# Kernel optimization log

Hardware: AMD Instinct MI355X
Metric: run time of the kernel (lower is better)

## Reference

```python
import jax, jax.numpy as jnp
import numpy as np

N_USERS = 65536
N_ENT = 8192
C = 64
N_REL = 16
E = 1000000
NNZ = 1000000
LAMBDA_COEFF = 0.5
EPS = 1e-12


def setup_inputs() -> dict:
    key = jax.random.key(0)
    ks = jax.random.split(key, 8)
    return {
        "user_emb": jax.random.normal(ks[0], (N_USERS, C), jnp.float32) * 0.1,
        "entity_emb": jax.random.normal(ks[1], (N_ENT, C), jnp.float32) * 0.1,
        "weight": jax.random.normal(ks[2], (N_REL - 1, C), jnp.float32) * 0.1,
        "edge_index": jax.random.randint(ks[3], (2, E), 0, N_ENT, dtype=jnp.int32),
        "edge_type": jax.random.randint(ks[4], (E,), 1, N_REL, dtype=jnp.int32),
        "interact_rows": jax.random.randint(ks[5], (NNZ,), 0, N_USERS, dtype=jnp.int32),
        "interact_cols": jax.random.randint(ks[6], (NNZ,), 0, N_ENT, dtype=jnp.int32),
        "interact_vals": jax.random.uniform(ks[7], (NNZ,), jnp.float32),
        "n_hops": 2,
        "topk": 10,
    }


def _l2_normalize(x):
    # F.normalize(p=2, dim=1) with eps=1e-12
    n = jnp.linalg.norm(x, axis=-1, keepdims=True)
    return x / jnp.maximum(n, EPS)


def _build_adj_dense(context, topk):
    # cosine-sim kNN graph + symmetric normalization, returned dense [n, n]
    n = context.shape[0]
    cn = context / jnp.linalg.norm(context, axis=-1, keepdims=True)
    sim = cn @ cn.T                                  # [n, n]
    knn_val, knn_ind = jax.lax.top_k(sim, topk)      # [n, k]
    rowsum = knn_val.sum(-1)                         # sparse rowsum per row
    d = rowsum ** -0.5                               # D^{-1/2}
    vals = d[:, None] * knn_val * d[knn_ind]         # D^-1/2 A D^-1/2 values
    rows = jnp.broadcast_to(jnp.arange(n)[:, None], (n, topk))
    return jnp.zeros((n, n), context.dtype).at[rows, knn_ind].add(vals)


def _aggregate(entity_emb, user_emb, head, tail, edge_type,
               interact_rows, interact_cols, interact_vals, weight):
    rel = weight[edge_type - 1]                      # [E, C]
    neigh = entity_emb[tail] * rel                   # [E, C]
    # per-edge attention: (||h*r||_2 * ||t*r||_2)^2  -> scalar per edge
    s = (jnp.linalg.norm(entity_emb[head] * rel, axis=1)
         * jnp.linalg.norm(neigh, axis=1)) ** 2      # [E]
    # scatter_softmax over edges grouped by head
    smax = jax.ops.segment_max(s, head, num_segments=N_ENT)
    ex = jnp.exp(s - smax[head])
    denom = jax.ops.segment_sum(ex, head, num_segments=N_ENT)
    w = ex / denom[head]                             # [E]
    entity_agg = jax.ops.segment_sum(neigh * w[:, None], head, num_segments=N_ENT)
    # user_agg = interact_mat @ entity_emb (sparse COO mm)
    user_agg = jax.ops.segment_sum(interact_vals[:, None] * entity_emb[interact_cols],
                                   interact_rows, num_segments=N_USERS)
    score = jax.nn.softmax(user_emb @ weight.T, axis=-1)   # [n_users, n_rel-1]
    user_agg = user_agg + (score @ weight) * user_agg
    return entity_agg, user_agg


def reference(user_emb, entity_emb, weight, edge_index, edge_type,
              interact_rows, interact_cols, interact_vals, n_hops, topk):
    head, tail = edge_index[0], edge_index[1]
    origin_item_adj = _build_adj_dense(entity_emb, topk)
    entity_res = entity_emb
    user_res = user_emb
    ent, usr = entity_emb, user_emb
    for _ in range(n_hops):
        ent, usr = _aggregate(ent, usr, head, tail, edge_type,
                              interact_rows, interact_cols, interact_vals, weight)
        ent = _l2_normalize(ent)
        usr = _l2_normalize(usr)
        entity_res = entity_res + ent
        user_res = user_res + usr
    item_adj = (1.0 - LAMBDA_COEFF) * _build_adj_dense(entity_res, topk) \
               + LAMBDA_COEFF * origin_item_adj
    return entity_res, user_res, item_adj
```

## Files before the change

### kernel.cpp

```cpp
#include <hip/hip_runtime.h>
#include <math.h>
#include <float.h>

#define N_USERS 65536
#define N_ENT   8192
#define CDIM    64
#define N_RELM1 15
#define E_EDGES 1000000
#define NNZV    1000000
#define TOPK    10
#define NCAND   12
#define EPSN    1e-12f

typedef float f32x4 __attribute__((ext_vector_type(4)));
typedef short short8 __attribute__((ext_vector_type(8)));

__device__ inline unsigned umaxu(unsigned a, unsigned b){ return a > b ? a : b; }
__device__ inline unsigned uminu(unsigned a, unsigned b){ return a < b ? a : b; }

__device__ inline float wred_sum(float v){
#pragma unroll
  for (int m = 32; m; m >>= 1) v += __shfl_xor(v, m, 64);
  return v;
}
__device__ inline float wred_max(float v){
#pragma unroll
  for (int m = 32; m; m >>= 1) v = fmaxf(v, __shfl_xor(v, m, 64));
  return v;
}

__device__ inline unsigned bf16_rne(float x){
  unsigned u = __float_as_uint(x);
  return (u + 0x7FFFu + ((u >> 16) & 1u)) >> 16;
}

__global__ __launch_bounds__(256) void k_prep(const float* __restrict__ x, float* __restrict__ cn,
                                              short* __restrict__ hi_p, short* __restrict__ lo_p,
                                              const float* __restrict__ wmat, float* __restrict__ nsq,
                                              int do_nsq){
  __shared__ float wl[N_RELM1 * CDIM];
  int tid = threadIdx.x;
  if (do_nsq){
    for (int t = tid; t < N_RELM1 * CDIM; t += 256) wl[t] = wmat[t];
  }
  __syncthreads();
  int w = blockIdx.x * 4 + (tid >> 6);
  int k = tid & 63;
  float v = x[w * CDIM + k];
  float ss = wred_sum(v * v);
  float cv = v / sqrtf(ss);
  cn[w * CDIM + k] = cv;
  unsigned h = bf16_rne(cv);
  float hf = __uint_as_float(h << 16);
  unsigned l2 = bf16_rne(cv - hf);
  int T = w >> 4, c = w & 15;
  int f = k >> 5, q = (k >> 3) & 3, j = k & 7;
  size_t a = ((size_t)(T * 2 + f) * 64 + q * 16 + c) * 8 + j;
  hi_p[a] = (short)h;
  lo_p[a] = (short)l2;
  if (do_nsq){
    float out = 0.f;
    for (int r = 0; r < N_RELM1; ++r){
      float t = v * wl[r * CDIM + k];
      float s2 = wred_sum(t * t);
      if (k == r) out = s2;
    }
    if (k < N_RELM1) nsq[w * N_RELM1 + k] = out;
  }
}

__global__ __launch_bounds__(256) void k_sim_topk(const short* __restrict__ hi_p,
                                                  const short* __restrict__ lo_p,
                                                  unsigned* __restrict__ keys){
  const int tid = threadIdx.x;
  const int w = tid >> 6, l = tid & 63;
  const int c = l & 15, q = l >> 4;
  const int rowset = (w >> 1) << 4;
  const int half = w & 1;
  const int cy = blockIdx.y;
  const int row0 = blockIdx.x * 32 + rowset;
  const int R = row0 >> 4;

  const short8* H8 = (const short8*)hi_p;
  const short8* L8 = (const short8*)lo_p;

  const short8 a_hi0 = H8[(size_t)R * 128 + l];
  const short8 a_hi1 = H8[(size_t)R * 128 + 64 + l];
  const short8 a_lo0 = L8[(size_t)R * 128 + l];
  const short8 a_lo1 = L8[(size_t)R * 128 + 64 + l];

  unsigned key[4][8];
#pragma unroll
  for (int s = 0; s < 4; ++s)
#pragma unroll
    for (int t = 0; t < 8; ++t) key[s][t] = 0u;

  const f32x4 z4 = {0.f, 0.f, 0.f, 0.f};
  const int bt = cy * 256 + half * 128;
#pragma unroll 2
  for (int lt = 0; lt < 128; ++lt){
    const size_t bo = (size_t)(bt + lt) * 128 + l;
    short8 b_hi0 = H8[bo];
    short8 b_hi1 = H8[bo + 64];
    short8 b_lo0 = L8[bo];
    short8 b_lo1 = L8[bo + 64];
    f32x4 p0 = __builtin_amdgcn_mfma_f32_16x16x32_bf16(a_hi0, b_hi0, z4, 0, 0, 0);
    f32x4 p1 = __builtin_amdgcn_mfma_f32_16x16x32_bf16(a_hi0, b_lo0, z4, 0, 0, 0);
    f32x4 p2 = __builtin_amdgcn_mfma_f32_16x16x32_bf16(a_lo0, b_hi0, z4, 0, 0, 0);
    p0 = __builtin_amdgcn_mfma_f32_16x16x32_bf16(a_hi1, b_hi1, p0, 0, 0, 0);
    p1 = __builtin_amdgcn_mfma_f32_16x16x32_bf16(a_hi1, b_lo1, p1, 0, 0, 0);
    p2 = __builtin_amdgcn_mfma_f32_16x16x32_bf16(a_lo1, b_hi1, p2, 0, 0, 0);
#pragma unroll
    for (int s = 0; s < 4; ++s){
      float v = p0[s] + p1[s] + p2[s];
      unsigned u = __float_as_uint(v);
      unsigned kk = ((u ^ (unsigned)(((int)u >> 31) | 0x80000000)) & 0xFFFFFF00u) | (unsigned)lt;
#pragma unroll
      for (int i = 7; i >= 1; --i)
        key[s][i] = umaxu(uminu(key[s][i - 1], kk), key[s][i]);
      key[s][0] = umaxu(key[s][0], kk);
    }
  }

#pragma unroll
  for (int s = 0; s < 4; ++s){
    int grow = row0 + 4 * q + s;
    unsigned* kp = keys + ((size_t)grow * 64 + (size_t)(cy * 32 + half * 16 + c)) * 8;
    ((uint4*)kp)[0] = (uint4){key[s][0], key[s][1], key[s][2], key[s][3]};
    ((uint4*)kp)[1] = (uint4){key[s][4], key[s][5], key[s][6], key[s][7]};
  }
}

__global__ __launch_bounds__(256) void k_refine(const float* __restrict__ cn,
                                                const unsigned* __restrict__ keys,
                                                float* __restrict__ kv, int* __restrict__ ki,
                                                float* __restrict__ dvec){
  int row = blockIdx.x * 4 + (threadIdx.x >> 6);
  int l = threadIdx.x & 63;
  const unsigned* kp = keys + ((size_t)row * 64 + l) * 8;
  uint4 k0 = ((const uint4*)kp)[0], k1 = ((const uint4*)kp)[1];
  unsigned kk0 = k0.x, kk1 = k0.y, kk2 = k0.z, kk3 = k0.w;
  unsigned kk4 = k1.x, kk5 = k1.y, kk6 = k1.z, kk7 = k1.w;
  const int cbase = (l >> 5) * 4096 + ((l >> 4) & 1) * 2048 + (l & 15);

  int ji[NCAND];
#pragma unroll
  for (int t = 0; t < NCAND; ++t){
    unsigned bk = kk0;
    int myc = cbase + (int)(kk0 & 0xFFu) * 16;
    int bc = myc;
#pragma unroll
    for (int m = 32; m; m >>= 1){
      unsigned ok = (unsigned)__shfl_xor((int)bk, m, 64);
      int oc = __shfl_xor(bc, m, 64);
      if (ok > bk || (ok == bk && oc < bc)){ bk = ok; bc = oc; }
    }
    if (kk0 == bk && myc == bc){
      kk0 = kk1; kk1 = kk2; kk2 = kk3; kk3 = kk4; kk4 = kk5; kk5 = kk6; kk6 = kk7; kk7 = 0u;
    }
    ji[t] = bc;
  }

  float v = cn[(size_t)row * CDIM + l];
  float dv[NCAND];
#pragma unroll
  for (int t = 0; t < NCAND; ++t)
    dv[t] = wred_sum(v * cn[(size_t)ji[t] * CDIM + l]);

  unsigned used = 0;
  float rs = 0.f;
  for (int k = 0; k < TOPK; ++k){
    float bv = -FLT_MAX; int bi = 0x7FFFFFFF; int bs = 0;
#pragma unroll
    for (int t = 0; t < NCAND; ++t){
      if (used & (1u << t)) continue;
      if (dv[t] > bv || (dv[t] == bv && ji[t] < bi)){ bv = dv[t]; bi = ji[t]; bs = t; }
    }
    used |= 1u << bs; rs += bv;
    if (l == 0){ kv[(size_t)row * TOPK + k] = bv; ki[(size_t)row * TOPK + k] = bi; }
  }
  if (l == 0) dvec[row] = 1.0f / sqrtf(rs);
}

__global__ void k_hist2(const int* __restrict__ head, const int* __restrict__ irows,
                        int* __restrict__ cnt_all){
  int e = blockIdx.x * blockDim.x + threadIdx.x;
  if (e < E_EDGES)                  atomicAdd(&cnt_all[head[e]], 1);
  else if (e < E_EDGES + NNZV)      atomicAdd(&cnt_all[N_ENT + irows[e - E_EDGES]], 1);
}

__global__ __launch_bounds__(1024) void k_scan_local2(const int* __restrict__ cnt_all,
                                                      int* __restrict__ rp_grp,
                                                      int* __restrict__ rp_int,
                                                      int* __restrict__ part){
  __shared__ int sh[1024];
  int b = blockIdx.x, tid = threadIdx.x;
  int src = (b < 8) ? (b * 1024 + tid) : (N_ENT + (b - 8) * 1024 + tid);
  int v = cnt_all[src];
  sh[tid] = v; __syncthreads();
  for (int off = 1; off < 1024; off <<= 1){
    int t = (tid >= off) ? sh[tid - off] : 0;
    __syncthreads();
    sh[tid] += t;
    __syncthreads();
  }
  int ex = sh[tid] - v;
  if (b < 8) rp_grp[b * 1024 + tid] = ex;
  else       rp_int[(b - 8) * 1024 + tid] = ex;
  if (tid == 1023) part[b] = sh[1023];
}

__global__ void k_scan_part2(int* __restrict__ part){
  int wid = threadIdx.x >> 6, lane = threadIdx.x & 63;
  if (wid == 0){
    int v = (lane < 8) ? part[lane] : 0;
    int orig = v;
    for (int off = 1; off < 64; off <<= 1){ int t = __shfl_up(v, off, 64); if (lane >= off) v += t; }
    if (lane < 8) part[lane] = v - orig;
  } else {
    int v = part[8 + lane];
    int orig = v;
    for (int off = 1; off < 64; off <<= 1){ int t = __shfl_up(v, off, 64); if (lane >= off) v += t; }
    part[8 + lane] = v - orig;
  }
}

__global__ __launch_bounds__(1024) void k_scan_add2(int* __restrict__ rp_grp, int* __restrict__ rp_int,
                                                    const int* __restrict__ part,
                                                    int* __restrict__ wk_grp, int* __restrict__ wk_int){
  int b = blockIdx.x, tid = threadIdx.x;
  if (b < 8){
    int g = b * 1024 + tid;
    int v = rp_grp[g] + part[b];
    rp_grp[g] = v; wk_grp[g] = v;
  } else {
    int g = (b - 8) * 1024 + tid;
    int v = rp_int[g] + part[b];
    rp_int[g] = v; wk_int[g] = v;
  }
  if (b == 0 && tid == 0){ rp_grp[N_ENT] = E_EDGES; rp_int[N_USERS] = NNZV; }
}

__global__ void k_scatter2(const int* __restrict__ head, const int* __restrict__ tail,
                           const int* __restrict__ etype,
                           const int* __restrict__ irows, const int* __restrict__ icols,
                           const float* __restrict__ ivals,
                           int* __restrict__ wk_grp, int* __restrict__ wk_int,
                           int* __restrict__ pack, int* __restrict__ ocol, float* __restrict__ oval){
  int e = blockIdx.x * blockDim.x + threadIdx.x;
  if (e < E_EDGES){
    int h = head[e];
    int pos = atomicAdd(&wk_grp[h], 1);
    pack[pos] = tail[e] | ((etype[e] - 1) << 16);
  } else if (e < E_EDGES + NNZV){
    int ee = e - E_EDGES;
    int r = irows[ee];
    int pos = atomicAdd(&wk_int[r], 1);
    ocol[pos] = icols[ee];
    oval[pos] = ivals[ee];
  }
}

__global__ __launch_bounds__(256) void k_entity_hop(const float* __restrict__ ent_cur,
                                                    const float* __restrict__ nsq,
                                                    const float* __restrict__ wmat,
                                                    const int* __restrict__ rowptr,
                                                    const int* __restrict__ pack,
                                                    float* __restrict__ ent_next,
                                                    float* __restrict__ nsq_next,
                                                    float* __restrict__ res, int hop0){
  __shared__ float wl[N_RELM1 * CDIM];
  int tid = threadIdx.x;
  for (int t = tid; t < N_RELM1 * CDIM; t += 256) wl[t] = wmat[t];
  __syncthreads();
  int i = blockIdx.x * 4 + (tid >> 6);
  int lane = tid & 63;
  int beg = rowptr[i], end = rowptr[i + 1];

  float sm = 0.f;
  for (int p = beg + lane; p < end; p += 64){
    int pk = pack[p]; int t = pk & 0xFFFF; int r = pk >> 16;
    sm = fmaxf(sm, nsq[i * N_RELM1 + r] * nsq[t * N_RELM1 + r]);
  }
  sm = wred_max(sm);

  float acc = 0.f, dsum = 0.f;
  for (int base = beg; base < end; base += 64){
    int p = base + lane;
    int pk = (p < end) ? pack[p] : 0;
    int t = pk & 0xFFFF; int r = pk >> 16;
    float s = nsq[i * N_RELM1 + r] * nsq[t * N_RELM1 + r];
    float e = (p < end) ? __expf(s - sm) : 0.f;
    dsum += e;
    int cnt = end - base; if (cnt > 64) cnt = 64;
#pragma unroll 8
    for (int qq = 0; qq < cnt; ++qq){
      float eq = __shfl(e, qq, 64);
      int tq = __shfl(t, qq, 64);
      int rq = __shfl(r, qq, 64);
      acc = fmaf(eq * wl[rq * CDIM + lane], ent_cur[(size_t)tq * CDIM + lane], acc);
    }
  }
  float denom = wred_sum(dsum);

  float agg = (end > beg) ? acc / denom : 0.f;
  float nrm = sqrtf(wred_sum(agg * agg));
  float out = agg / fmaxf(nrm, EPSN);
  if (hop0){
    ent_next[(size_t)i * CDIM + lane] = out;
    res[(size_t)i * CDIM + lane] = ent_cur[(size_t)i * CDIM + lane] + out;
    float o = 0.f;
    for (int r = 0; r < N_RELM1; ++r){
      float t = out * wl[r * CDIM + lane];
      float s2 = wred_sum(t * t);
      if (lane == r) o = s2;
    }
    if (lane < N_RELM1) nsq_next[i * N_RELM1 + lane] = o;
  } else {
    res[(size_t)i * CDIM + lane] += out;
  }
}

__global__ __launch_bounds__(256) void k_user_hop(const float* __restrict__ base,
                                                  const float* __restrict__ ent_cur,
                                                  const float* __restrict__ wmat,
                                                  const int* __restrict__ rowptr,
                                                  const int* __restrict__ cols,
                                                  const float* __restrict__ vals,
                                                  float* __restrict__ res, int hop0){
  __shared__ float wl[N_RELM1 * CDIM];
  int tid = threadIdx.x;
  for (int t = tid; t < N_RELM1 * CDIM; t += 256) wl[t] = wmat[t];
  __syncthreads();
  int u = blockIdx.x * 4 + (tid >> 6);
  int lane = tid & 63;
  float bv = base[(size_t)u * CDIM + lane];
  float rprev = hop0 ? bv : res[(size_t)u * CDIM + lane];
  float uv = hop0 ? bv : (rprev - bv);

  float dr[N_RELM1];
#pragma unroll
  for (int r = 0; r < N_RELM1; ++r) dr[r] = wred_sum(uv * wl[r * CDIM + lane]);
  float mx = dr[0];
#pragma unroll
  for (int r = 1; r < N_RELM1; ++r) mx = fmaxf(mx, dr[r]);
  float se = 0.f;
#pragma unroll
  for (int r = 0; r < N_RELM1; ++r){ dr[r] = __expf(dr[r] - mx); se += dr[r]; }
  float m = 0.f;
#pragma unroll
  for (int r = 0; r < N_RELM1; ++r) m = fmaf(dr[r], wl[r * CDIM + lane], m);
  m /= se;

  int beg = rowptr[u], end = rowptr[u + 1];
  float acc = 0.f;
#pragma unroll 4
  for (int p = beg; p < end; ++p)
    acc = fmaf(vals[p], ent_cur[(size_t)cols[p] * CDIM + lane], acc);

  float u2 = acc * (1.f + m);
  float nrm = sqrtf(wred_sum(u2 * u2));
  float out = u2 / fmaxf(nrm, EPSN);
  res[(size_t)u * CDIM + lane] = rprev + out;
}

__global__ void k_scatter_adj2(const float* __restrict__ kv0, const int* __restrict__ ki0,
                               const float* __restrict__ d0,
                               const float* __restrict__ kv2, const int* __restrict__ ki2,
                               const float* __restrict__ d2,
                               float* __restrict__ adj){
  int g = blockIdx.x * blockDim.x + threadIdx.x;
  const int n = N_ENT * TOPK;
  if (g < n){
    int i = g / TOPK; int j = ki0[g];
    atomicAdd(&adj[(size_t)i * N_ENT + j], 0.5f * d0[i] * kv0[g] * d0[j]);
  } else if (g < 2 * n){
    int gg = g - n;
    int i = gg / TOPK; int j = ki2[gg];
    atomicAdd(&adj[(size_t)i * N_ENT + j], 0.5f * d2[i] * kv2[gg] * d2[j]);
  }
}

extern "C" void kernel_launch(void* const* d_in, const int* in_sizes, int n_in,
                              void* d_out, int out_size, void* d_ws, size_t ws_size,
                              hipStream_t stream){
  const float* user_emb   = (const float*)d_in[0];
  const float* entity_emb = (const float*)d_in[1];
  const float* weight     = (const float*)d_in[2];
  const int*   head       = (const int*)d_in[3];
  const int*   tail       = head + E_EDGES;
  const int*   etype      = (const int*)d_in[4];
  const int*   irows      = (const int*)d_in[5];
  const int*   icols      = (const int*)d_in[6];
  const float* ivals      = (const float*)d_in[7];

  float* out_ent = (float*)d_out;
  float* out_usr = out_ent + (size_t)N_ENT * CDIM;
  float* out_adj = out_usr + (size_t)N_USERS * CDIM;

  char* W = (char*)d_ws;
  size_t off = 0;
  auto alloc = [&](size_t bytes) -> char* {
    char* p = W + off;
    off = (off + bytes + 1023) & ~(size_t)1023;
    return p;
  };
  float* cn       = (float*)alloc((size_t)N_ENT * CDIM * 4);
  short* cn_hi    = (short*)alloc((size_t)N_ENT * CDIM * 2);
  short* cn_lo    = (short*)alloc((size_t)N_ENT * CDIM * 2);
  unsigned* skeys = (unsigned*)alloc((size_t)N_ENT * 64 * 8 * 4);
  float* kv0      = (float*)alloc((size_t)N_ENT * TOPK * 4);
  int*   ki0      = (int*)  alloc((size_t)N_ENT * TOPK * 4);
  float* kv2      = (float*)alloc((size_t)N_ENT * TOPK * 4);
  int*   ki2      = (int*)  alloc((size_t)N_ENT * TOPK * 4);
  float* d0       = (float*)alloc((size_t)N_ENT * 4);
  float* d2       = (float*)alloc((size_t)N_ENT * 4);
  float* nsq_a    = (float*)alloc((size_t)N_ENT * N_RELM1 * 4);
  float* nsq_b    = (float*)alloc((size_t)N_ENT * N_RELM1 * 4);
  float* ent_a    = (float*)alloc((size_t)N_ENT * CDIM * 4);
  int*   cnt_all  = (int*)  alloc((size_t)(N_ENT + N_USERS) * 4);
  int*   rp_grp   = (int*)  alloc((size_t)(N_ENT + 1) * 4);
  int*   wk_grp   = (int*)  alloc((size_t)N_ENT * 4);
  int*   grp_pack = (int*)  alloc((size_t)E_EDGES * 4);
  int*   rp_int   = (int*)  alloc((size_t)(N_USERS + 1) * 4);
  int*   wk_int   = (int*)  alloc((size_t)N_USERS * 4);
  int*   int_col  = (int*)  alloc((size_t)NNZV * 4);
  float* int_val  = (float*)alloc((size_t)NNZV * 4);
  int*   part     = (int*)  alloc(128 * 4);

  const int TOT = E_EDGES + NNZV;
  const int TB  = (TOT + 255) / 256;

  hipMemsetAsync(cnt_all, 0, (size_t)(N_ENT + N_USERS) * 4, stream);
  k_hist2<<<TB, 256, 0, stream>>>(head, irows, cnt_all);
  k_scan_local2<<<72, 1024, 0, stream>>>(cnt_all, rp_grp, rp_int, part);
  k_scan_part2<<<1, 128, 0, stream>>>(part);
  k_scan_add2<<<72, 1024, 0, stream>>>(rp_grp, rp_int, part, wk_grp, wk_int);
  k_scatter2<<<TB, 256, 0, stream>>>(head, tail, etype, irows, icols, ivals,
                                     wk_grp, wk_int, grp_pack, int_col, int_val);

  k_prep<<<N_ENT / 4, 256, 0, stream>>>(entity_emb, cn, cn_hi, cn_lo, weight, nsq_a, 1);
  k_sim_topk<<<dim3(N_ENT / 32, 2), 256, 0, stream>>>(cn_hi, cn_lo, skeys);
  k_refine<<<N_ENT / 4, 256, 0, stream>>>(cn, skeys, kv0, ki0, d0);

  k_entity_hop<<<N_ENT / 4, 256, 0, stream>>>(entity_emb, nsq_a, weight, rp_grp, grp_pack,
                                              ent_a, nsq_b, out_ent, 1);
  k_user_hop<<<N_USERS / 4, 256, 0, stream>>>(user_emb, entity_emb, weight, rp_int,
                                              int_col, int_val, out_usr, 1);

  k_entity_hop<<<N_ENT / 4, 256, 0, stream>>>(ent_a, nsq_b, weight, rp_grp, grp_pack,
                                              ent_a, nsq_b, out_ent, 0);
  k_user_hop<<<N_USERS / 4, 256, 0, stream>>>(user_emb, ent_a, weight, rp_int,
                                              int_col, int_val, out_usr, 0);

  k_prep<<<N_ENT / 4, 256, 0, stream>>>(out_ent, cn, cn_hi, cn_lo, weight, nsq_a, 0);
  k_sim_topk<<<dim3(N_ENT / 32, 2), 256, 0, stream>>>(cn_hi, cn_lo, skeys);
  k_refine<<<N_ENT / 4, 256, 0, stream>>>(cn, skeys, kv2, ki2, d2);

  hipMemsetAsync(out_adj, 0, (size_t)N_ENT * N_ENT * 4, stream);
  k_scatter_adj2<<<(2 * N_ENT * TOPK + 255) / 256, 256, 0, stream>>>(kv0, ki0, d0, kv2, ki2, d2, out_adj);
}
```

Measured before the change: 1.032 ms.

## Use single-bf16 similarity, privatized histogram/scatter counters, and fused adjacency zero-write

The candidate similarity screen now uses one bf16 MFMA product instead of the three-term hi/lo split, and the exact fp32 refine pass widens from 12 to 16 candidates to make up for the lower screening precision. The edge/interaction histogram and scatter atomics are spread over 8 block-indexed counter copies to cut atomic contention, with the scan extended to produce per-copy cursors. The separate memset plus scatter kernel for the dense adjacency is replaced by one kernel per row that zeroes the row and then adds its top-k entries. The risk is that a true top-10 neighbour falls outside the 16 bf16-ranked candidates.

```diff
diff --git a/kernel.cpp b/kernel.cpp
--- a/kernel.cpp
+++ b/kernel.cpp
@@ -9,7 +9,8 @@
 #define E_EDGES 1000000
 #define NNZV    1000000
 #define TOPK    10
-#define NCAND   12
+#define NCAND   16
+#define KTOT    (N_ENT + N_USERS)
 #define EPSN    1e-12f
 
 typedef float f32x4 __attribute__((ext_vector_type(4)));
@@ -35,7 +36,7 @@
 }
 
 __global__ __launch_bounds__(256) void k_prep(const float* __restrict__ x, float* __restrict__ cn,
-                                              short* __restrict__ hi_p, short* __restrict__ lo_p,
+                                              short* __restrict__ hi_p,
                                               const float* __restrict__ wmat, float* __restrict__ nsq,
                                               int do_nsq){
   __shared__ float wl[N_RELM1 * CDIM];
@@ -51,13 +52,10 @@
   float cv = v / sqrtf(ss);
   cn[w * CDIM + k] = cv;
   unsigned h = bf16_rne(cv);
-  float hf = __uint_as_float(h << 16);
-  unsigned l2 = bf16_rne(cv - hf);
   int T = w >> 4, c = w & 15;
   int f = k >> 5, q = (k >> 3) & 3, j = k & 7;
   size_t a = ((size_t)(T * 2 + f) * 64 + q * 16 + c) * 8 + j;
   hi_p[a] = (short)h;
-  lo_p[a] = (short)l2;
   if (do_nsq){
     float out = 0.f;
     for (int r = 0; r < N_RELM1; ++r){
@@ -70,7 +68,6 @@
 }
 
 __global__ __launch_bounds__(256) void k_sim_topk(const short* __restrict__ hi_p,
-                                                  const short* __restrict__ lo_p,
                                                   unsigned* __restrict__ keys){
   const int tid = threadIdx.x;
   const int w = tid >> 6, l = tid & 63;
@@ -82,12 +79,9 @@
   const int R = row0 >> 4;
 
   const short8* H8 = (const short8*)hi_p;
-  const short8* L8 = (const short8*)lo_p;
 
   const short8 a_hi0 = H8[(size_t)R * 128 + l];
   const short8 a_hi1 = H8[(size_t)R * 128 + 64 + l];
-  const short8 a_lo0 = L8[(size_t)R * 128 + l];
-  const short8 a_lo1 = L8[(size_t)R * 128 + 64 + l];
 
   unsigned key[4][8];
 #pragma unroll
@@ -102,17 +96,11 @@
     const size_t bo = (size_t)(bt + lt) * 128 + l;
     short8 b_hi0 = H8[bo];
     short8 b_hi1 = H8[bo + 64];
-    short8 b_lo0 = L8[bo];
-    short8 b_lo1 = L8[bo + 64];
     f32x4 p0 = __builtin_amdgcn_mfma_f32_16x16x32_bf16(a_hi0, b_hi0, z4, 0, 0, 0);
-    f32x4 p1 = __builtin_amdgcn_mfma_f32_16x16x32_bf16(a_hi0, b_lo0, z4, 0, 0, 0);
-    f32x4 p2 = __builtin_amdgcn_mfma_f32_16x16x32_bf16(a_lo0, b_hi0, z4, 0, 0, 0);
     p0 = __builtin_amdgcn_mfma_f32_16x16x32_bf16(a_hi1, b_hi1, p0, 0, 0, 0);
-    p1 = __builtin_amdgcn_mfma_f32_16x16x32_bf16(a_hi1, b_lo1, p1, 0, 0, 0);
-    p2 = __builtin_amdgcn_mfma_f32_16x16x32_bf16(a_lo1, b_hi1, p2, 0, 0, 0);
 #pragma unroll
     for (int s = 0; s < 4; ++s){
-      float v = p0[s] + p1[s] + p2[s];
+      float v = p0[s];
       unsigned u = __float_as_uint(v);
       unsigned kk = ((u ^ (unsigned)(((int)u >> 31) | 0x80000000)) & 0xFFFFFF00u) | (unsigned)lt;
 #pragma unroll
@@ -182,35 +170,42 @@
   if (l == 0) dvec[row] = 1.0f / sqrtf(rs);
 }
 
-__global__ void k_hist2(const int* __restrict__ head, const int* __restrict__ irows,
-                        int* __restrict__ cnt_all){
+__global__ void k_hist8(const int* __restrict__ head, const int* __restrict__ irows,
+                        int* __restrict__ cnt8){
   int e = blockIdx.x * blockDim.x + threadIdx.x;
-  if (e < E_EDGES)                  atomicAdd(&cnt_all[head[e]], 1);
-  else if (e < E_EDGES + NNZV)      atomicAdd(&cnt_all[N_ENT + irows[e - E_EDGES]], 1);
-}
-
-__global__ __launch_bounds__(1024) void k_scan_local2(const int* __restrict__ cnt_all,
+  int s = blockIdx.x & 7;
+  if (e < E_EDGES)             atomicAdd(&cnt8[s * KTOT + head[e]], 1);
+  else if (e < E_EDGES + NNZV) atomicAdd(&cnt8[s * KTOT + N_ENT + irows[e - E_EDGES]], 1);
+}
+
+__global__ __launch_bounds__(1024) void k_scan_local8(const int* __restrict__ cnt8,
                                                       int* __restrict__ rp_grp,
                                                       int* __restrict__ rp_int,
+                                                      int* __restrict__ cur8,
                                                       int* __restrict__ part){
   __shared__ int sh[1024];
   int b = blockIdx.x, tid = threadIdx.x;
-  int src = (b < 8) ? (b * 1024 + tid) : (N_ENT + (b - 8) * 1024 + tid);
-  int v = cnt_all[src];
-  sh[tid] = v; __syncthreads();
+  int keyidx = b * 1024 + tid;
+  int c[8]; int tot = 0;
+#pragma unroll
+  for (int s = 0; s < 8; ++s){ c[s] = cnt8[s * KTOT + keyidx]; tot += c[s]; }
+  sh[tid] = tot; __syncthreads();
   for (int off = 1; off < 1024; off <<= 1){
     int t = (tid >= off) ? sh[tid - off] : 0;
     __syncthreads();
     sh[tid] += t;
     __syncthreads();
   }
-  int ex = sh[tid] - v;
-  if (b < 8) rp_grp[b * 1024 + tid] = ex;
-  else       rp_int[(b - 8) * 1024 + tid] = ex;
+  int ex = sh[tid] - tot;
+  if (keyidx < N_ENT) rp_grp[keyidx] = ex;
+  else                rp_int[keyidx - N_ENT] = ex;
+  int run = ex;
+#pragma unroll
+  for (int s = 0; s < 8; ++s){ cur8[s * KTOT + keyidx] = run; run += c[s]; }
   if (tid == 1023) part[b] = sh[1023];
 }
 
-__global__ void k_scan_part2(int* __restrict__ part){
+__global__ void k_scan_part8(int* __restrict__ part){
   int wid = threadIdx.x >> 6, lane = threadIdx.x & 63;
   if (wid == 0){
     int v = (lane < 8) ? part[lane] : 0;
@@ -225,37 +220,35 @@
   }
 }
 
-__global__ __launch_bounds__(1024) void k_scan_add2(int* __restrict__ rp_grp, int* __restrict__ rp_int,
-                                                    const int* __restrict__ part,
-                                                    int* __restrict__ wk_grp, int* __restrict__ wk_int){
+__global__ __launch_bounds__(1024) void k_scan_add8(int* __restrict__ rp_grp, int* __restrict__ rp_int,
+                                                    int* __restrict__ cur8,
+                                                    const int* __restrict__ part){
   int b = blockIdx.x, tid = threadIdx.x;
-  if (b < 8){
-    int g = b * 1024 + tid;
-    int v = rp_grp[g] + part[b];
-    rp_grp[g] = v; wk_grp[g] = v;
-  } else {
-    int g = (b - 8) * 1024 + tid;
-    int v = rp_int[g] + part[b];
-    rp_int[g] = v; wk_int[g] = v;
-  }
+  int keyidx = b * 1024 + tid;
+  int p = part[b];
+  if (keyidx < N_ENT) rp_grp[keyidx] += p;
+  else                rp_int[keyidx - N_ENT] += p;
+#pragma unroll
+  for (int s = 0; s < 8; ++s) cur8[s * KTOT + keyidx] += p;
   if (b == 0 && tid == 0){ rp_grp[N_ENT] = E_EDGES; rp_int[N_USERS] = NNZV; }
 }
 
-__global__ void k_scatter2(const int* __restrict__ head, const int* __restrict__ tail,
+__global__ void k_scatter8(const int* __restrict__ head, const int* __restrict__ tail,
                            const int* __restrict__ etype,
                            const int* __restrict__ irows, const int* __restrict__ icols,
                            const float* __restrict__ ivals,
-                           int* __restrict__ wk_grp, int* __restrict__ wk_int,
+                           int* __restrict__ cur8,
                            int* __restrict__ pack, int* __restrict__ ocol, float* __restrict__ oval){
   int e = blockIdx.x * blockDim.x + threadIdx.x;
+  int s = blockIdx.x & 7;
   if (e < E_EDGES){
     int h = head[e];
-    int pos = atomicAdd(&wk_grp[h], 1);
+    int pos = atomicAdd(&cur8[s * KTOT + h], 1);
     pack[pos] = tail[e] | ((etype[e] - 1) << 16);
   } else if (e < E_EDGES + NNZV){
     int ee = e - E_EDGES;
     int r = irows[ee];
-    int pos = atomicAdd(&wk_int[r], 1);
+    int pos = atomicAdd(&cur8[s * KTOT + N_ENT + r], 1);
     ocol[pos] = icols[ee];
     oval[pos] = ivals[ee];
   }
@@ -364,20 +357,25 @@
   res[(size_t)u * CDIM + lane] = rprev + out;
 }
 
-__global__ void k_scatter_adj2(const float* __restrict__ kv0, const int* __restrict__ ki0,
-                               const float* __restrict__ d0,
-                               const float* __restrict__ kv2, const int* __restrict__ ki2,
-                               const float* __restrict__ d2,
-                               float* __restrict__ adj){
-  int g = blockIdx.x * blockDim.x + threadIdx.x;
-  const int n = N_ENT * TOPK;
-  if (g < n){
-    int i = g / TOPK; int j = ki0[g];
-    atomicAdd(&adj[(size_t)i * N_ENT + j], 0.5f * d0[i] * kv0[g] * d0[j]);
-  } else if (g < 2 * n){
-    int gg = g - n;
-    int i = gg / TOPK; int j = ki2[gg];
-    atomicAdd(&adj[(size_t)i * N_ENT + j], 0.5f * d2[i] * kv2[gg] * d2[j]);
+__global__ __launch_bounds__(256) void k_adj_write(const float* __restrict__ kv0, const int* __restrict__ ki0,
+                                                   const float* __restrict__ d0,
+                                                   const float* __restrict__ kv2, const int* __restrict__ ki2,
+                                                   const float* __restrict__ d2,
+                                                   float* __restrict__ adj){
+  int i = blockIdx.x;
+  int tid = threadIdx.x;
+  float4* rowp = (float4*)(adj + (size_t)i * N_ENT);
+  const float4 z = {0.f, 0.f, 0.f, 0.f};
+#pragma unroll
+  for (int k = 0; k < 8; ++k) rowp[k * 256 + tid] = z;
+  __syncthreads();
+  if (tid < TOPK){
+    int j = ki0[i * TOPK + tid];
+    atomicAdd(&adj[(size_t)i * N_ENT + j], 0.5f * d0[i] * kv0[i * TOPK + tid] * d0[j]);
+  } else if (tid < 2 * TOPK){
+    int t = tid - TOPK;
+    int j = ki2[i * TOPK + t];
+    atomicAdd(&adj[(size_t)i * N_ENT + j], 0.5f * d2[i] * kv2[i * TOPK + t] * d2[j]);
   }
 }
 
@@ -407,7 +405,6 @@
   };
   float* cn       = (float*)alloc((size_t)N_ENT * CDIM * 4);
   short* cn_hi    = (short*)alloc((size_t)N_ENT * CDIM * 2);
-  short* cn_lo    = (short*)alloc((size_t)N_ENT * CDIM * 2);
   unsigned* skeys = (unsigned*)alloc((size_t)N_ENT * 64 * 8 * 4);
   float* kv0      = (float*)alloc((size_t)N_ENT * TOPK * 4);
   int*   ki0      = (int*)  alloc((size_t)N_ENT * TOPK * 4);
@@ -418,12 +415,11 @@
   float* nsq_a    = (float*)alloc((size_t)N_ENT * N_RELM1 * 4);
   float* nsq_b    = (float*)alloc((size_t)N_ENT * N_RELM1 * 4);
   float* ent_a    = (float*)alloc((size_t)N_ENT * CDIM * 4);
-  int*   cnt_all  = (int*)  alloc((size_t)(N_ENT + N_USERS) * 4);
+  int*   cnt8     = (int*)  alloc((size_t)8 * KTOT * 4);
+  int*   cur8     = (int*)  alloc((size_t)8 * KTOT * 4);
   int*   rp_grp   = (int*)  alloc((size_t)(N_ENT + 1) * 4);
-  int*   wk_grp   = (int*)  alloc((size_t)N_ENT * 4);
   int*   grp_pack = (int*)  alloc((size_t)E_EDGES * 4);
   int*   rp_int   = (int*)  alloc((size_t)(N_USERS + 1) * 4);
-  int*   wk_int   = (int*)  alloc((size_t)N_USERS * 4);
   int*   int_col  = (int*)  alloc((size_t)NNZV * 4);
   float* int_val  = (float*)alloc((size_t)NNZV * 4);
   int*   part     = (int*)  alloc(128 * 4);
@@ -431,16 +427,16 @@
   const int TOT = E_EDGES + NNZV;
   const int TB  = (TOT + 255) / 256;
 
-  hipMemsetAsync(cnt_all, 0, (size_t)(N_ENT + N_USERS) * 4, stream);
-  k_hist2<<<TB, 256, 0, stream>>>(head, irows, cnt_all);
-  k_scan_local2<<<72, 1024, 0, stream>>>(cnt_all, rp_grp, rp_int, part);
-  k_scan_part2<<<1, 128, 0, stream>>>(part);
-  k_scan_add2<<<72, 1024, 0, stream>>>(rp_grp, rp_int, part, wk_grp, wk_int);
-  k_scatter2<<<TB, 256, 0, stream>>>(head, tail, etype, irows, icols, ivals,
-                                     wk_grp, wk_int, grp_pack, int_col, int_val);
-
-  k_prep<<<N_ENT / 4, 256, 0, stream>>>(entity_emb, cn, cn_hi, cn_lo, weight, nsq_a, 1);
-  k_sim_topk<<<dim3(N_ENT / 32, 2), 256, 0, stream>>>(cn_hi, cn_lo, skeys);
+  hipMemsetAsync(cnt8, 0, (size_t)8 * KTOT * 4, stream);
+  k_hist8<<<TB, 256, 0, stream>>>(head, irows, cnt8);
+  k_scan_local8<<<KTOT / 1024, 1024, 0, stream>>>(cnt8, rp_grp, rp_int, cur8, part);
+  k_scan_part8<<<1, 128, 0, stream>>>(part);
+  k_scan_add8<<<KTOT / 1024, 1024, 0, stream>>>(rp_grp, rp_int, cur8, part);
+  k_scatter8<<<TB, 256, 0, stream>>>(head, tail, etype, irows, icols, ivals,
+                                     cur8, grp_pack, int_col, int_val);
+
+  k_prep<<<N_ENT / 4, 256, 0, stream>>>(entity_emb, cn, cn_hi, weight, nsq_a, 1);
+  k_sim_topk<<<dim3(N_ENT / 32, 2), 256, 0, stream>>>(cn_hi, skeys);
   k_refine<<<N_ENT / 4, 256, 0, stream>>>(cn, skeys, kv0, ki0, d0);
 
   k_entity_hop<<<N_ENT / 4, 256, 0, stream>>>(entity_emb, nsq_a, weight, rp_grp, grp_pack,
@@ -453,10 +449,9 @@
   k_user_hop<<<N_USERS / 4, 256, 0, stream>>>(user_emb, ent_a, weight, rp_int,
                                               int_col, int_val, out_usr, 0);
 
-  k_prep<<<N_ENT / 4, 256, 0, stream>>>(out_ent, cn, cn_hi, cn_lo, weight, nsq_a, 0);
-  k_sim_topk<<<dim3(N_ENT / 32, 2), 256, 0, stream>>>(cn_hi, cn_lo, skeys);
+  k_prep<<<N_ENT / 4, 256, 0, stream>>>(out_ent, cn, cn_hi, weight, nsq_a, 0);
+  k_sim_topk<<<dim3(N_ENT / 32, 2), 256, 0, stream>>>(cn_hi, skeys);
   k_refine<<<N_ENT / 4, 256, 0, stream>>>(cn, skeys, kv2, ki2, d2);
 
-  hipMemsetAsync(out_adj, 0, (size_t)N_ENT * N_ENT * 4, stream);
-  k_scatter_adj2<<<(2 * N_ENT * TOPK + 255) / 256, 256, 0, stream>>>(kv0, ki0, d0, kv2, ki2, d2, out_adj);
-}
+  k_adj_write<<<N_ENT, 256, 0, stream>>>(kv0, ki0, d0, kv2, ki2, d2, out_adj);
+}
```

Result: no change. 1.026 ms (-0.5%).
